# Kernel optimization log

Hardware: AMD Instinct MI355X
Metric: run time of the kernel (lower is better)

## Reference

```python
import jax, jax.numpy as jnp
import numpy as np

B, S, SE, D, H = 4, 1024, 256, 1536, 24
HD = D // H
EPS = 1e-5
STYLE_IDX = np.array([0, 0, 2, 2])  # expand_first: style stats of sample 0 -> {0,1}, sample 2 -> {2,3}


def adain(feat):
    # feat: [B,H,S,hd]; stats over seq dim (-2), unbiased var like torch
    m = feat.mean(axis=-2, keepdims=True)
    s = jnp.sqrt(feat.var(axis=-2, keepdims=True, ddof=1) + EPS)
    sm, ss = m[STYLE_IDX], s[STYLE_IDX]
    styled = (feat - m) / s * ss + sm
    # only batch indices 1 and 3 are restyled
    mask = jnp.array([0.0, 1.0, 0.0, 1.0], dtype=feat.dtype).reshape(B, 1, 1, 1)
    return feat * (1.0 - mask) + styled * mask


def heads(x):
    b, s, _ = x.shape
    return x.reshape(b, s, H, HD).transpose(0, 2, 1, 3)


def setup_inputs() -> dict:
    key = jax.random.key(0)
    ks = jax.random.split(key, 12)
    w = lambda k: jax.random.normal(k, (D, D), dtype=jnp.float32) * 0.02
    z = jnp.zeros((D,), dtype=jnp.float32)
    return {
        'hidden_states': jax.random.normal(ks[0], (B, S, D), dtype=jnp.float32),
        'encoder_hidden_states': jax.random.normal(ks[1], (B, SE, D), dtype=jnp.float32),
        'wq': w(ks[2]), 'bq': z, 'wk': w(ks[3]), 'bk': z, 'wv': w(ks[4]), 'bv': z,
        'awq': w(ks[5]), 'abq': z, 'awk': w(ks[6]), 'abk': z, 'awv': w(ks[7]), 'abv': z,
        'wo': w(ks[8]), 'bo': z, 'wao': w(ks[9]), 'bao': z,
    }


def reference(hidden_states, encoder_hidden_states, wq, bq, wk, bk, wv, bv,
              awq, abq, awk, abk, awv, abv, wo, bo, wao, bao):
    q = heads(hidden_states @ wq + bq)   # [B,H,S,hd]
    k = heads(hidden_states @ wk + bk)
    v = heads(hidden_states @ wv + bv)
    # adain_queries / adain_keys (adain_values=False)
    q = adain(q)
    k = adain(k)
    # share_attention: concat style K/V (scale=1.0 -> plain expand) along seq
    k = jnp.concatenate([k, k[STYLE_IDX]], axis=2)  # [B,H,2S,hd]
    v = jnp.concatenate([v, v[STYLE_IDX]], axis=2)
    # joint (text) streams
    eq = heads(encoder_hidden_states @ awq + abq)
    ek = heads(encoder_hidden_states @ awk + abk)
    ev = heads(encoder_hidden_states @ awv + abv)
    q = jnp.concatenate([q, eq], axis=2)   # [B,H,S+SE,hd]
    k = jnp.concatenate([k, ek], axis=2)   # [B,H,2S+SE,hd]
    v = jnp.concatenate([v, ev], axis=2)
    scale = 1.0 / np.sqrt(HD)
    logits = jnp.einsum('bhqd,bhkd->bhqk', q, k) * scale
    probs = jax.nn.softmax(logits, axis=-1)
    out = jnp.einsum('bhqk,bhkd->bhqd', probs, v)
    out = out.transpose(0, 2, 1, 3).reshape(B, -1, D)
    hid, enc = out[:, :S], out[:, S:]
    hid = hid @ wo + bo            # to_out[0] (to_out[1] is dropout/identity)
    enc = enc @ wao + bao          # to_add_out (context_pre_only=False)
    return hid, enc
```

## Files before the change

### kernel.cpp

```cpp
#include <hip/hip_runtime.h>
#include <hip/hip_bf16.h>


#define NB 4
#define NS 1024
#define NSE 256
#define ND 1536
#define NH 24
#define LK2 1280
#define SMAX 20.0f

typedef short bf16x8 __attribute__((ext_vector_type(8)));
typedef float f32x4 __attribute__((ext_vector_type(4)));

struct WPtrs { const float* w[8]; };
struct B6    { const float* p[6]; };

__device__ __forceinline__ unsigned short f2bf(float x) {
  union { float f; unsigned u; } a; a.f = x;
  unsigned r = a.u + 0x7fffu + ((a.u >> 16) & 1u);
  return (unsigned short)(r >> 16);
}
__device__ __forceinline__ void split2(float x, unsigned short& h, unsigned short& l) {
  union { float f; unsigned u; } a; a.f = x;
  h = (unsigned short)(a.u >> 16);
  union { float f; unsigned u; } b; b.u = a.u & 0xffff0000u;
  union { float f; unsigned u; } c; c.f = x - b.f;
  l = (unsigned short)(c.u >> 16);
}

__device__ __forceinline__ void gload_lds16(const unsigned short* g, unsigned short* l) {
  __builtin_amdgcn_global_load_lds(
      (const __attribute__((address_space(1))) void*)g,
      (__attribute__((address_space(3))) void*)l, 16, 0, 0);
}

__global__ __launch_bounds__(256) void conv_split_all(
    const float* __restrict__ hs, const float* __restrict__ ehs,
    unsigned short* __restrict__ HSh, unsigned short* __restrict__ HSl,
    unsigned short* __restrict__ EHh, unsigned short* __restrict__ EHl)
{
  int i = blockIdx.x * 256 + threadIdx.x;
  const float4* src; ushort4 *dh, *dl; int j;
  if (i < 1572864) { src = (const float4*)hs; j = i; dh = (ushort4*)HSh; dl = (ushort4*)HSl; }
  else { j = i - 1572864; src = (const float4*)ehs; dh = (ushort4*)EHh; dl = (ushort4*)EHl; }
  float4 v = src[j];
  ushort4 h, lo;
  split2(v.x, h.x, lo.x); split2(v.y, h.y, lo.y);
  split2(v.z, h.z, lo.z); split2(v.w, h.w, lo.w);
  dh[j] = h; dl[j] = lo;
}

__global__ __launch_bounds__(256) void conv_wt_all(WPtrs wp,
                                                   unsigned short* __restrict__ Wsp)
{
  __shared__ float tile[32][33];
  const int z = blockIdx.z;
  const float* W = wp.w[z];
  unsigned short* Th = Wsp + (long)(2 * z) * 2359296;
  unsigned short* Tl = Th + 2359296;
  const int k0 = blockIdx.x * 32, n0 = blockIdx.y * 32;
  const int r = threadIdx.x >> 5, c = threadIdx.x & 31;
#pragma unroll
  for (int i = 0; i < 4; ++i)
    tile[r + 8 * i][c] = W[(long)(k0 + r + 8 * i) * ND + n0 + c];
  __syncthreads();
#pragma unroll
  for (int i = 0; i < 4; ++i) {
    float v = tile[c][r + 8 * i];
    long o = (long)(n0 + r + 8 * i) * ND + k0 + c;
    unsigned short h, l;
    split2(v, h, l);
    Th[o] = h; Tl[o] = l;
  }
}

__device__ __forceinline__ void gemm_mfma_body(
    const unsigned short* __restrict__ Ah, const unsigned short* __restrict__ Al,
    const unsigned short* __restrict__ Bh, const unsigned short* __restrict__ Bl,
    const float* __restrict__ bias, float* __restrict__ C, int m0, int n0,
    bool third)
{
  __shared__ unsigned short sAh[128 * 32], sAl[128 * 32];
  __shared__ unsigned short sBh[128 * 32], sBl[128 * 32];

  const int t = threadIdx.x;
  const int w = t >> 6, l = t & 63;

  const int lr = l >> 2;
  const int lc = (l & 3) * 8;

  const unsigned short* pAh = Ah + (long)(m0 + 32 * w + lr) * ND + lc;
  const unsigned short* pAl = Al + (long)(m0 + 32 * w + lr) * ND + lc;
  const unsigned short* pBh = Bh + (long)(n0 + 32 * w + lr) * ND + lc;
  const unsigned short* pBl = Bl + (long)(n0 + 32 * w + lr) * ND + lc;

  unsigned short* qAh0 = &sAh[(32 * w) * 32];
  unsigned short* qAh1 = &sAh[(32 * w + 16) * 32];
  unsigned short* qAl0 = &sAl[(32 * w) * 32];
  unsigned short* qAl1 = &sAl[(32 * w + 16) * 32];
  unsigned short* qBh0 = &sBh[(32 * w) * 32];
  unsigned short* qBh1 = &sBh[(32 * w + 16) * 32];
  unsigned short* qBl0 = &sBl[(32 * w) * 32];
  unsigned short* qBl1 = &sBl[(32 * w + 16) * 32];

  const int rowA = (w >> 1) * 64 + (l & 15);
  const int rowB = (w & 1) * 64 + (l & 15);
  const int ko = (l >> 4) * 8;

  f32x4 acc[4][4] = {};

  for (int k0 = 0; k0 < ND; k0 += 32) {
    gload_lds16(pAh, qAh0);
    gload_lds16(pAh + 16 * ND, qAh1);
    if (third) {
      gload_lds16(pAl, qAl0);
      gload_lds16(pAl + 16 * ND, qAl1);
    }
    gload_lds16(pBh, qBh0);
    gload_lds16(pBh + 16 * ND, qBh1);
    gload_lds16(pBl, qBl0);
    gload_lds16(pBl + 16 * ND, qBl1);
    pAh += 32; pAl += 32; pBh += 32; pBl += 32;
    __syncthreads();

    bf16x8 fah[4], fal[4], fbh[4], fbl[4];
#pragma unroll
    for (int mt = 0; mt < 4; ++mt)
      fah[mt] = *(const bf16x8*)&sAh[(rowA + mt * 16) * 32 + ko];
    if (third) {
#pragma unroll
      for (int mt = 0; mt < 4; ++mt)
        fal[mt] = *(const bf16x8*)&sAl[(rowA + mt * 16) * 32 + ko];
    }
#pragma unroll
    for (int nt = 0; nt < 4; ++nt) {
      fbh[nt] = *(const bf16x8*)&sBh[(rowB + nt * 16) * 32 + ko];
      fbl[nt] = *(const bf16x8*)&sBl[(rowB + nt * 16) * 32 + ko];
    }
#pragma unroll
    for (int mt = 0; mt < 4; ++mt)
#pragma unroll
      for (int nt = 0; nt < 4; ++nt) {
        acc[mt][nt] = __builtin_amdgcn_mfma_f32_16x16x32_bf16(fah[mt], fbh[nt], acc[mt][nt], 0, 0, 0);
        acc[mt][nt] = __builtin_amdgcn_mfma_f32_16x16x32_bf16(fah[mt], fbl[nt], acc[mt][nt], 0, 0, 0);
      }
    if (third) {
#pragma unroll
      for (int mt = 0; mt < 4; ++mt)
#pragma unroll
        for (int nt = 0; nt < 4; ++nt)
          acc[mt][nt] = __builtin_amdgcn_mfma_f32_16x16x32_bf16(fal[mt], fbh[nt], acc[mt][nt], 0, 0, 0);
    }
    __syncthreads();
  }

  const int col0 = n0 + (w & 1) * 64 + (l & 15);
  const int row0 = m0 + (w >> 1) * 64 + (l >> 4) * 4;
#pragma unroll
  for (int nt = 0; nt < 4; ++nt) {
    float bv = bias[col0 + nt * 16];
#pragma unroll
    for (int mt = 0; mt < 4; ++mt)
#pragma unroll
      for (int r = 0; r < 4; ++r)
        C[(long)(row0 + mt * 16 + r) * ND + col0 + nt * 16] = acc[mt][nt][r] + bv;
  }
}

__global__ __launch_bounds__(256) void gemm3_all(
    const unsigned short* __restrict__ HSh, const unsigned short* __restrict__ HSl,
    const unsigned short* __restrict__ EHh, const unsigned short* __restrict__ EHl,
    const unsigned short* __restrict__ Wsp, B6 biases,
    float* __restrict__ Qb, float* __restrict__ EQb)
{
  const int z = blockIdx.z, y = blockIdx.y;
  const unsigned short *Ah, *Al;
  float* C;
  int m0, widx;
  if (y < 32) { Ah = HSh; Al = HSl; m0 = y * 128; widx = z;
                C = Qb + (long)z * 6291456; }
  else        { Ah = EHh; Al = EHl; m0 = (y - 32) * 128; widx = 3 + z;
                C = EQb + (long)z * 1572864; }
  const unsigned short* Bh = Wsp + (long)(2 * widx) * 2359296;
  const unsigned short* Bl = Bh + 2359296;
  gemm_mfma_body(Ah, Al, Bh, Bl, biases.p[widx], C, m0, blockIdx.x * 128,
                 z == 2);
}

__global__ __launch_bounds__(256) void gemm_out_all(
    const unsigned short* __restrict__ AOh,
    const unsigned short* __restrict__ Wsp,
    const float* __restrict__ bo, const float* __restrict__ bao,
    float* __restrict__ out)
{
  const int z = blockIdx.z, y = blockIdx.y;
  const unsigned short *Ah, *Bh, *Bl;
  const float* bias;
  float* C;
  int m0;
  if (y < 8) {
    Ah = AOh + (long)z * 1966080;
    m0 = y * 128;
    Bh = Wsp + (long)12 * 2359296; Bl = Bh + 2359296;
    bias = bo; C = out + (long)z * 1572864;
  } else {
    Ah = AOh + 1572864 + (long)z * 1966080;
    m0 = (y - 8) * 128;
    Bh = Wsp + (long)14 * 2359296; Bl = Bh + 2359296;
    bias = bao; C = out + 6291456 + (long)z * 393216;
  }
  gemm_mfma_body(Ah, Ah, Bh, Bl, bias, C, m0, blockIdx.x * 128, false);
}

__global__ __launch_bounds__(256) void adain_stats2(
    const float* __restrict__ Qb, const float* __restrict__ Kb,
    float* __restrict__ stm, float* __restrict__ sts,
    float* __restrict__ stm2, float* __restrict__ sts2)
{
  const float* X = blockIdx.z ? Kb : Qb;
  float* meanb = blockIdx.z ? stm2 : stm;
  float* sigb  = blockIdx.z ? sts2 : sts;
  const int b  = blockIdx.x;
  const int t  = threadIdx.x;
  const int dl = t & 63;
  const int sg = t >> 6;
  const int d  = blockIdx.y * 64 + dl;
  const float* xp = X + (long)b * NS * ND + d;
  float sum = 0.f, sq = 0.f;
  for (int s = sg; s < NS; s += 4) {
    float v = xp[(long)s * ND];
    sum += v; sq += v * v;
  }
  __shared__ float ss[4][64], s2[4][64];
  ss[sg][dl] = sum; s2[sg][dl] = sq;
  __syncthreads();
  if (t < 64) {
    float tot = ss[0][t] + ss[1][t] + ss[2][t] + ss[3][t];
    float tq  = s2[0][t] + s2[1][t] + s2[2][t] + s2[3][t];
    float mean = tot * (1.f / 1024.f);
    float var  = (tq - tot * mean) * (1.f / 1023.f);
    meanb[b * ND + blockIdx.y * 64 + t] = mean;
    sigb [b * ND + blockIdx.y * 64 + t] = sqrtf(var + 1e-5f);
  }
}

__global__ __launch_bounds__(256) void conv_KV(
    const float* __restrict__ Kf, const float* __restrict__ EKf,
    const float* __restrict__ Vf, const float* __restrict__ EVf,
    const float* __restrict__ stm2, const float* __restrict__ sts2,
    unsigned short* __restrict__ Kh, unsigned short* __restrict__ Kl,
    unsigned short* __restrict__ VT)
{
  __shared__ float tile[64][65];
  const int bh = blockIdx.y, b = bh / NH, h = bh - b * NH;
  if (blockIdx.x < 20) {
    const int key = blockIdx.x * 64 + (threadIdx.x >> 2);
    const int dc = (threadIdx.x & 3) * 16;
    const bool kad = ((b & 1) != 0) && (key < NS);
    const int srcb = b & 2;
    const float* src = (key < NS)
        ? Kf  + ((long)b * NS + key) * ND + h * 64 + dc
        : EKf + ((long)b * NSE + key - NS) * ND + h * 64 + dc;
    unsigned short* dh = Kh + ((long)bh * LK2 + key) * 64 + dc;
    unsigned short* dl = Kl + ((long)bh * LK2 + key) * 64 + dc;
    const long sb = (long)b * ND + h * 64 + dc;
    const long ss = (long)srcb * ND + h * 64 + dc;
#pragma unroll
    for (int i = 0; i < 4; ++i) {
      float4 v = *(const float4*)(src + 4 * i);
      if (kad) {
        float4 mb = *(const float4*)(stm2 + sb + 4 * i);
        float4 gb = *(const float4*)(sts2 + sb + 4 * i);
        float4 ms = *(const float4*)(stm2 + ss + 4 * i);
        float4 gs = *(const float4*)(sts2 + ss + 4 * i);
        v.x = (v.x - mb.x) * (gs.x / gb.x) + ms.x;
        v.y = (v.y - mb.y) * (gs.y / gb.y) + ms.y;
        v.z = (v.z - mb.z) * (gs.z / gb.z) + ms.z;
        v.w = (v.w - mb.w) * (gs.w / gb.w) + ms.w;
      }
      ushort4 hi, lo;
      split2(v.x, hi.x, lo.x); split2(v.y, hi.y, lo.y);
      split2(v.z, hi.z, lo.z); split2(v.w, hi.w, lo.w);
      *(ushort4*)(dh + 4 * i) = hi;
      *(ushort4*)(dl + 4 * i) = lo;
    }
  } else {
    const int k0 = (blockIdx.x - 20) * 64;
    {
      const int kl_ = threadIdx.x >> 2, dc = (threadIdx.x & 3) * 16;
      const int key = k0 + kl_;
      const float* src = (key < NS)
          ? Vf  + ((long)b * NS + key) * ND + h * 64 + dc
          : EVf + ((long)b * NSE + key - NS) * ND + h * 64 + dc;
#pragma unroll
      for (int i = 0; i < 4; ++i) {
        float4 v = *(const float4*)(src + 4 * i);
        tile[kl_][dc + 4 * i + 0] = v.x; tile[kl_][dc + 4 * i + 1] = v.y;
        tile[kl_][dc + 4 * i + 2] = v.z; tile[kl_][dc + 4 * i + 3] = v.w;
      }
    }
    __syncthreads();
    const int d = threadIdx.x >> 2, kc = (threadIdx.x & 3) * 16;
    unsigned short* dst = VT + ((long)bh * 64 + d) * LK2 + k0 + kc;
#pragma unroll
    for (int i = 0; i < 4; ++i) {
      ushort4 o4;
      o4.x = f2bf(tile[kc + 4 * i + 0][d]);
      o4.y = f2bf(tile[kc + 4 * i + 1][d]);
      o4.z = f2bf(tile[kc + 4 * i + 2][d]);
      o4.w = f2bf(tile[kc + 4 * i + 3][d]);
      *(ushort4*)(dst + 4 * i) = o4;
    }
  }
}

__global__ __launch_bounds__(256) void attn_mfma(
    const float* __restrict__ Q, const float* __restrict__ EQ,
    const unsigned short* __restrict__ Khg, const unsigned short* __restrict__ Klg,
    const unsigned short* __restrict__ VTg,
    const float* __restrict__ stm, const float* __restrict__ sts,
    unsigned short* __restrict__ AOh)
{
  __shared__ unsigned short sKh[2][64 * 64], sKl[2][64 * 64], sVT[2][64 * 64];
  __shared__ unsigned short sPh[64 * 72], sPl[64 * 72];

  const int t = threadIdx.x, w = t >> 6, l = t & 63;
  const int bh = blockIdx.y, b = bh / NH, h = bh - b * NH;
  const int bhs = (b & 2) * NH + h;
  const int q0 = blockIdx.x * 64;
  const int m = l & 15, g = l >> 4;
  const bool beven = (b & 1) == 0;
  const int nIter = beven ? 20 : 36;

  union FU { bf16x8 v; unsigned short u[8]; };
  FU qh[2], ql[2];
  {
    const bool qad = !beven && (q0 < NS);
    const int srcb = b & 2;
    const float* qrow = (q0 < NS)
        ? (Q  + ((long)b * NS + q0 + 16 * w + m) * ND + h * 64)
        : (EQ + ((long)b * NSE + (q0 - NS) + 16 * w + m) * ND + h * 64);
#pragma unroll
    for (int ks = 0; ks < 2; ++ks) {
      const int d0 = h * 64 + ks * 32 + g * 8;
      const float* p = qrow + ks * 32 + g * 8;
      float4 v0 = *(const float4*)p, v1 = *(const float4*)(p + 4);
      float vv[8] = {v0.x, v0.y, v0.z, v0.w, v1.x, v1.y, v1.z, v1.w};
      if (qad) {
        float4 mb0 = *(const float4*)(stm + (long)b * ND + d0);
        float4 mb1 = *(const float4*)(stm + (long)b * ND + d0 + 4);
        float4 gb0 = *(const float4*)(sts + (long)b * ND + d0);
        float4 gb1 = *(const float4*)(sts + (long)b * ND + d0 + 4);
        float4 ms0 = *(const float4*)(stm + (long)srcb * ND + d0);
        float4 ms1 = *(const float4*)(stm + (long)srcb * ND + d0 + 4);
        float4 gs0 = *(const float4*)(sts + (long)srcb * ND + d0);
        float4 gs1 = *(const float4*)(sts + (long)srcb * ND + d0 + 4);
        float mb[8] = {mb0.x, mb0.y, mb0.z, mb0.w, mb1.x, mb1.y, mb1.z, mb1.w};
        float gb[8] = {gb0.x, gb0.y, gb0.z, gb0.w, gb1.x, gb1.y, gb1.z, gb1.w};
        float ms[8] = {ms0.x, ms0.y, ms0.z, ms0.w, ms1.x, ms1.y, ms1.z, ms1.w};
        float gs[8] = {gs0.x, gs0.y, gs0.z, gs0.w, gs1.x, gs1.y, gs1.z, gs1.w};
#pragma unroll
        for (int j = 0; j < 8; ++j)
          vv[j] = (vv[j] - mb[j]) * (gs[j] / gb[j]) + ms[j];
      }
#pragma unroll
      for (int j = 0; j < 8; ++j)
        split2(vv[j] * 0.125f, qh[ks].u[j], ql[ks].u[j]);
    }
  }

  const int srow = l >> 3;
  const int sp = l & 7;
  const int osw = (sp - srow) & 7;
  const long ownK = (long)bh * LK2 * 64, styK = (long)bhs * LK2 * 64;
  const long ownV = (long)bh * 64 * LK2, styV = (long)bhs * 64 * LK2;
  const int offK = (16 * w + srow) * 64 + osw * 8;
  const int offV = (16 * w + srow) * LK2 + osw * 8;

  auto stage = [&](int kt, int bi) {
    int zone, j;
    if (beven) { zone = (kt < 16) ? 0 : 2; j = (kt < 16) ? kt : kt - 16; }
    else {
      zone = (kt < 16) ? 0 : ((kt < 32) ? 1 : 2);
      j = (kt < 16) ? kt : ((kt < 32) ? kt - 16 : kt - 32);
    }
    const long keyBase = ((zone == 2) ? 1024 : 0) + (long)j * 64;
    const unsigned short* kb = Khg + ((zone == 1) ? styK : ownK) + keyBase * 64;
    const unsigned short* lb = Klg + ((zone == 1) ? styK : ownK) + keyBase * 64;
    const unsigned short* vb = VTg + ((zone == 1) ? styV : ownV) + keyBase;
    gload_lds16(kb + offK, &sKh[bi][(16 * w) * 64]);
    gload_lds16(kb + 8 * 64 + offK, &sKh[bi][(16 * w + 8) * 64]);
    gload_lds16(lb + offK, &sKl[bi][(16 * w) * 64]);
    gload_lds16(lb + 8 * 64 + offK, &sKl[bi][(16 * w + 8) * 64]);
    gload_lds16(vb + offV, &sVT[bi][(16 * w) * 64]);
    gload_lds16(vb + 8 * LK2 + offV, &sVT[bi][(16 * w + 8) * 64]);
  };

  const int p0 = (g + m) & 7;
  const int p1 = (4 + g + m) & 7;

  f32x4 oacc[4] = {};
  float l_part[4] = {0.f, 0.f, 0.f, 0.f};

  stage(0, 0);

  for (int kt = 0; kt < nIter; ++kt) {
    const int cur = kt & 1;
    __syncthreads();
    if (kt + 1 < nIter) stage(kt + 1, cur ^ 1);

    const float ebias = (beven && kt < 16) ? (0.69314718f - SMAX) : (-SMAX);

    f32x4 sacc[4] = {};
#pragma unroll
    for (int ks = 0; ks < 2; ++ks) {
      const int pp = ks ? p1 : p0;
#pragma unroll
      for (int nt = 0; nt < 4; ++nt) {
        const int ak = (nt * 16 + m) * 64 + pp * 8;
        bf16x8 fkh = *(const bf16x8*)&sKh[cur][ak];
        bf16x8 fkl = *(const bf16x8*)&sKl[cur][ak];
        sacc[nt] = __builtin_amdgcn_mfma_f32_16x16x32_bf16(qh[ks].v, fkh, sacc[nt], 0, 0, 0);
        sacc[nt] = __builtin_amdgcn_mfma_f32_16x16x32_bf16(qh[ks].v, fkl, sacc[nt], 0, 0, 0);
        sacc[nt] = __builtin_amdgcn_mfma_f32_16x16x32_bf16(ql[ks].v, fkh, sacc[nt], 0, 0, 0);
      }
    }

#pragma unroll
    for (int nt = 0; nt < 4; ++nt)
#pragma unroll
      for (int r = 0; r < 4; ++r)
        sacc[nt][r] = __expf(sacc[nt][r] + ebias);
#pragma unroll
    for (int r = 0; r < 4; ++r)
      l_part[r] += (sacc[0][r] + sacc[1][r]) + (sacc[2][r] + sacc[3][r]);
#pragma unroll
    for (int nt = 0; nt < 4; ++nt)
#pragma unroll
      for (int r = 0; r < 4; ++r) {
        unsigned short ph, pl;
        split2(sacc[nt][r], ph, pl);
        const int ad = (16 * w + 4 * g + r) * 72 + nt * 16 + m;
        sPh[ad] = ph; sPl[ad] = pl;
      }

#pragma unroll
    for (int ks = 0; ks < 2; ++ks) {
      const int pp = ks ? p1 : p0;
      const int ap = (16 * w + m) * 72 + ks * 32 + g * 8;
      bf16x8 fph = *(const bf16x8*)&sPh[ap];
      bf16x8 fpl = *(const bf16x8*)&sPl[ap];
#pragma unroll
      for (int nt2 = 0; nt2 < 4; ++nt2) {
        const int av = (nt2 * 16 + m) * 64 + pp * 8;
        bf16x8 fv = *(const bf16x8*)&sVT[cur][av];
        oacc[nt2] = __builtin_amdgcn_mfma_f32_16x16x32_bf16(fph, fv, oacc[nt2], 0, 0, 0);
        oacc[nt2] = __builtin_amdgcn_mfma_f32_16x16x32_bf16(fpl, fv, oacc[nt2], 0, 0, 0);
      }
    }
  }

#pragma unroll
  for (int r = 0; r < 4; ++r) {
#pragma unroll
    for (int off = 1; off < 16; off <<= 1)
      l_part[r] += __shfl_xor(l_part[r], off, 16);
  }
#pragma unroll
  for (int r = 0; r < 4; ++r) {
    float inv = 1.f / l_part[r];
    const long row = (long)b * 1280 + q0 + 16 * w + 4 * g + r;
    const long base = row * ND + h * 64;
#pragma unroll
    for (int nt2 = 0; nt2 < 4; ++nt2)
      AOh[base + nt2 * 16 + m] = f2bf(oacc[nt2][r] * inv);
  }
}

extern "C" void kernel_launch(void* const* d_in, const int* in_sizes, int n_in,
                              void* d_out, int out_size, void* d_ws, size_t ws_size,
                              hipStream_t stream) {
  const float* hs  = (const float*)d_in[0];
  const float* ehs = (const float*)d_in[1];
  WPtrs wp;
  wp.w[0] = (const float*)d_in[2];  wp.w[1] = (const float*)d_in[4];
  wp.w[2] = (const float*)d_in[6];  wp.w[3] = (const float*)d_in[8];
  wp.w[4] = (const float*)d_in[10]; wp.w[5] = (const float*)d_in[12];
  wp.w[6] = (const float*)d_in[14]; wp.w[7] = (const float*)d_in[16];
  B6 biases;
  biases.p[0] = (const float*)d_in[3];
  biases.p[1] = (const float*)d_in[5];
  biases.p[2] = (const float*)d_in[7];
  biases.p[3] = (const float*)d_in[9];
  biases.p[4] = (const float*)d_in[11];
  biases.p[5] = (const float*)d_in[13];
  const float* bo  = (const float*)d_in[15];
  const float* bao = (const float*)d_in[17];
  float* out = (float*)d_out;

  float* Qb  = (float*)d_ws;
  float* Kb  = Qb  + 6291456;
  float* Vb  = Kb  + 6291456;
  float* EQb = Vb  + 6291456;
  float* EKb = EQb + 1572864;
  float* EVb = EKb + 1572864;
  float* stm  = EVb + 1572864;
  float* sts  = stm + 6144;
  float* stm2 = sts + 6144;
  float* sts2 = stm2 + 6144;
  unsigned short* U0  = (unsigned short*)(sts2 + 6144);
  unsigned short* HSh = U0;
  unsigned short* HSl = U0 + 6291456;
  unsigned short* EHh = U0 + 12582912;
  unsigned short* EHl = U0 + 14155776;
  unsigned short* AOh = U0;
  unsigned short* Wsp = U0 + 15728640;
  unsigned short* Khg = Wsp;
  unsigned short* Klg = Wsp + 7864320;
  unsigned short* VTg = Wsp + 15728640;

  dim3 blk(256);

  conv_split_all<<<7680, blk, 0, stream>>>(hs, ehs, HSh, HSl, EHh, EHl);
  conv_wt_all<<<dim3(48, 48, 8), blk, 0, stream>>>(wp, Wsp);

  gemm3_all<<<dim3(12, 40, 3), blk, 0, stream>>>(
      HSh, HSl, EHh, EHl, Wsp, biases, Qb, EQb);

  adain_stats2<<<dim3(4, 24, 2), blk, 0, stream>>>(Qb, Kb, stm, sts, stm2, sts2);

  conv_KV<<<dim3(40, 96), blk, 0, stream>>>(Kb, EKb, Vb, EVb, stm2, sts2,
                                            Khg, Klg, VTg);

  attn_mfma<<<dim3(20, 96), blk, 0, stream>>>(Qb, EQb, Khg, Klg, VTg,
                                              stm, sts, AOh);

  gemm_out_all<<<dim3(12, 10, 4), blk, 0, stream>>>(AOh, Wsp, bo, bao, out);
}
```

Before: 740.3 us.

## Load V fragments directly to registers, remap blocks, use exp2 and setprio

The attention kernel now reads V^T fragments straight from global memory into registers instead of staging them through LDS. This shrinks shared memory use and allows a launch bound of 3 blocks per CU. The grid is flattened and remapped so consecutive blocks are spread across heads, likely for XCD/L2 locality. The 1/sqrt(d) scale is folded with log2(e) so the kernel can call exp2 directly. s_setprio is raised around the MFMA sections. The direct global V loads are issued before each tile's compute and may add latency if they are not hidden.

```diff
diff --git a/kernel.cpp b/kernel.cpp
--- a/kernel.cpp
+++ b/kernel.cpp
@@ -9,6 +9,7 @@
 #define NH 24
 #define LK2 1280
 #define SMAX 20.0f
+#define LOG2E 1.44269504f
 
 typedef short bf16x8 __attribute__((ext_vector_type(8)));
 typedef float f32x4 __attribute__((ext_vector_type(4)));
@@ -315,20 +316,23 @@
   }
 }
 
-__global__ __launch_bounds__(256) void attn_mfma(
+__global__ __launch_bounds__(256, 3) void attn_mfma(
     const float* __restrict__ Q, const float* __restrict__ EQ,
     const unsigned short* __restrict__ Khg, const unsigned short* __restrict__ Klg,
     const unsigned short* __restrict__ VTg,
     const float* __restrict__ stm, const float* __restrict__ sts,
     unsigned short* __restrict__ AOh)
 {
-  __shared__ unsigned short sKh[2][64 * 64], sKl[2][64 * 64], sVT[2][64 * 64];
+  __shared__ unsigned short sKh[2][64 * 64], sKl[2][64 * 64];
   __shared__ unsigned short sPh[64 * 72], sPl[64 * 72];
 
   const int t = threadIdx.x, w = t >> 6, l = t & 63;
-  const int bh = blockIdx.y, b = bh / NH, h = bh - b * NH;
+  const int lin = blockIdx.x;
+  const int idx = (lin & 7) * 240 + (lin >> 3);
+  const int bh = idx / 20;
+  const int q0 = (idx % 20) * 64;
+  const int b = bh / NH, h = bh - b * NH;
   const int bhs = (b & 2) * NH + h;
-  const int q0 = blockIdx.x * 64;
   const int m = l & 15, g = l >> 4;
   const bool beven = (b & 1) == 0;
   const int nIter = beven ? 20 : 36;
@@ -366,7 +370,7 @@
       }
 #pragma unroll
       for (int j = 0; j < 8; ++j)
-        split2(vv[j] * 0.125f, qh[ks].u[j], ql[ks].u[j]);
+        split2(vv[j] * (0.125f * LOG2E), qh[ks].u[j], ql[ks].u[j]);
     }
   }
 
@@ -376,9 +380,8 @@
   const long ownK = (long)bh * LK2 * 64, styK = (long)bhs * LK2 * 64;
   const long ownV = (long)bh * 64 * LK2, styV = (long)bhs * 64 * LK2;
   const int offK = (16 * w + srow) * 64 + osw * 8;
-  const int offV = (16 * w + srow) * LK2 + osw * 8;
-
-  auto stage = [&](int kt, int bi) {
+
+  auto kvoff = [&](int kt, long& kOff, long& vOff) {
     int zone, j;
     if (beven) { zone = (kt < 16) ? 0 : 2; j = (kt < 16) ? kt : kt - 16; }
     else {
@@ -386,19 +389,24 @@
       j = (kt < 16) ? kt : ((kt < 32) ? kt - 16 : kt - 32);
     }
     const long keyBase = ((zone == 2) ? 1024 : 0) + (long)j * 64;
-    const unsigned short* kb = Khg + ((zone == 1) ? styK : ownK) + keyBase * 64;
-    const unsigned short* lb = Klg + ((zone == 1) ? styK : ownK) + keyBase * 64;
-    const unsigned short* vb = VTg + ((zone == 1) ? styV : ownV) + keyBase;
+    kOff = ((zone == 1) ? styK : ownK) + keyBase * 64;
+    vOff = ((zone == 1) ? styV : ownV) + keyBase;
+  };
+
+  auto stage = [&](int kt, int bi) {
+    long kOff, vOff;
+    kvoff(kt, kOff, vOff);
+    const unsigned short* kb = Khg + kOff;
+    const unsigned short* lb = Klg + kOff;
     gload_lds16(kb + offK, &sKh[bi][(16 * w) * 64]);
     gload_lds16(kb + 8 * 64 + offK, &sKh[bi][(16 * w + 8) * 64]);
     gload_lds16(lb + offK, &sKl[bi][(16 * w) * 64]);
     gload_lds16(lb + 8 * 64 + offK, &sKl[bi][(16 * w + 8) * 64]);
-    gload_lds16(vb + offV, &sVT[bi][(16 * w) * 64]);
-    gload_lds16(vb + 8 * LK2 + offV, &sVT[bi][(16 * w + 8) * 64]);
   };
 
   const int p0 = (g + m) & 7;
   const int p1 = (4 + g + m) & 7;
+  const long vlane = (long)m * LK2 + g * 8;
 
   f32x4 oacc[4] = {};
   float l_part[4] = {0.f, 0.f, 0.f, 0.f};
@@ -408,11 +416,24 @@
   for (int kt = 0; kt < nIter; ++kt) {
     const int cur = kt & 1;
     __syncthreads();
+
+    long kOff, vOff;
+    kvoff(kt, kOff, vOff);
+    const unsigned short* vb = VTg + vOff + vlane;
+    bf16x8 fvr[2][4];
+#pragma unroll
+    for (int ks = 0; ks < 2; ++ks)
+#pragma unroll
+      for (int nt2 = 0; nt2 < 4; ++nt2)
+        fvr[ks][nt2] = *(const bf16x8*)(vb + (long)nt2 * (16 * LK2) + ks * 32);
+
     if (kt + 1 < nIter) stage(kt + 1, cur ^ 1);
 
-    const float ebias = (beven && kt < 16) ? (0.69314718f - SMAX) : (-SMAX);
+    const float ebias = (beven && kt < 16) ? (1.0f - SMAX * LOG2E)
+                                           : (-SMAX * LOG2E);
 
     f32x4 sacc[4] = {};
+    __builtin_amdgcn_s_setprio(1);
 #pragma unroll
     for (int ks = 0; ks < 2; ++ks) {
       const int pp = ks ? p1 : p0;
@@ -426,12 +447,13 @@
         sacc[nt] = __builtin_amdgcn_mfma_f32_16x16x32_bf16(ql[ks].v, fkh, sacc[nt], 0, 0, 0);
       }
     }
+    __builtin_amdgcn_s_setprio(0);
 
 #pragma unroll
     for (int nt = 0; nt < 4; ++nt)
 #pragma unroll
       for (int r = 0; r < 4; ++r)
-        sacc[nt][r] = __expf(sacc[nt][r] + ebias);
+        sacc[nt][r] = __builtin_amdgcn_exp2f(sacc[nt][r] + ebias);
 #pragma unroll
     for (int r = 0; r < 4; ++r)
       l_part[r] += (sacc[0][r] + sacc[1][r]) + (sacc[2][r] + sacc[3][r]);
@@ -445,20 +467,19 @@
         sPh[ad] = ph; sPl[ad] = pl;
       }
 
+    __builtin_amdgcn_s_setprio(1);
 #pragma unroll
     for (int ks = 0; ks < 2; ++ks) {
-      const int pp = ks ? p1 : p0;
       const int ap = (16 * w + m) * 72 + ks * 32 + g * 8;
       bf16x8 fph = *(const bf16x8*)&sPh[ap];
       bf16x8 fpl = *(const bf16x8*)&sPl[ap];
 #pragma unroll
       for (int nt2 = 0; nt2 < 4; ++nt2) {
-        const int av = (nt2 * 16 + m) * 64 + pp * 8;
-        bf16x8 fv = *(const bf16x8*)&sVT[cur][av];
-        oacc[nt2] = __builtin_amdgcn_mfma_f32_16x16x32_bf16(fph, fv, oacc[nt2], 0, 0, 0);
-        oacc[nt2] = __builtin_amdgcn_mfma_f32_16x16x32_bf16(fpl, fv, oacc[nt2], 0, 0, 0);
-      }
-    }
+        oacc[nt2] = __builtin_amdgcn_mfma_f32_16x16x32_bf16(fph, fvr[ks][nt2], oacc[nt2], 0, 0, 0);
+        oacc[nt2] = __builtin_amdgcn_mfma_f32_16x16x32_bf16(fpl, fvr[ks][nt2], oacc[nt2], 0, 0, 0);
+      }
+    }
+    __builtin_amdgcn_s_setprio(0);
   }
 
 #pragma unroll
@@ -533,8 +554,8 @@
   conv_KV<<<dim3(40, 96), blk, 0, stream>>>(Kb, EKb, Vb, EVb, stm2, sts2,
                                             Khg, Klg, VTg);
 
-  attn_mfma<<<dim3(20, 96), blk, 0, stream>>>(Qb, EQb, Khg, Klg, VTg,
-                                              stm, sts, AOh);
+  attn_mfma<<<dim3(1920), blk, 0, stream>>>(Qb, EQb, Khg, Klg, VTg,
+                                            stm, sts, AOh);
 
   gemm_out_all<<<dim3(12, 10, 4), blk, 0, stream>>>(AOh, Wsp, bo, bao, out);
 }
```

Result: slower. 824.4 us (+11.4%).
